# Kernel optimization log

Measured on AMD Instinct MI355X. Metric: run time of the kernel, lower is better.

The kernel has to match this reference:

```python
import jax, jax.numpy as jnp
import numpy as np

DIM = 2048
RANK = 128


def _xavier_uniform(key, shape, gain=0.5):
    fan_out, fan_in = shape
    limit = gain * np.sqrt(6.0 / (fan_in + fan_out))
    return jax.random.uniform(key, shape, jnp.float32, -limit, limit)


def setup_inputs() -> dict:
    key = jax.random.key(0)
    ks = jax.random.split(key, 6)
    T, B = 1024, 16
    x = jax.random.normal(ks[0], (T, B, DIM), jnp.float32)
    h0 = jax.random.normal(ks[1], (B, DIM), jnp.float32)
    U_x = _xavier_uniform(ks[2], (DIM, RANK))
    V_x = _xavier_uniform(ks[3], (RANK, DIM))
    U_d = _xavier_uniform(ks[4], (DIM, RANK))
    V_d = _xavier_uniform(ks[5], (RANK, DIM))
    r_h = jnp.full((DIM,), 0.9, jnp.float32)
    r_delta = jnp.full((DIM,), 0.1, jnp.float32)
    b = jnp.zeros((DIM,), jnp.float32)
    b_delta = jnp.full((DIM,), -2.0, jnp.float32)
    b_gate = jnp.zeros((DIM,), jnp.float32)
    return {"x": x, "h0": h0, "U_x": U_x, "V_x": V_x, "U_d": U_d, "V_d": V_d,
            "r_h": r_h, "r_delta": r_delta, "b": b, "b_delta": b_delta, "b_gate": b_gate}


def reference(x, h0, U_x, V_x, U_d, V_d, r_h, r_delta, b, b_delta, b_gate):
    # Precompute input projections for all timesteps (batched low-rank GEMMs):
    # W(x) = U @ (V @ x)  ->  [T,B,D]
    wx = jnp.einsum('tbd,rd,or->tbo', x, V_x, U_x)
    wd = jnp.einsum('tbd,rd,or->tbo', x, V_d, U_d)

    def step(h_prev, inp):
        x_t, wx_t, wd_t = inp
        cand = jnp.tanh(r_h * h_prev + wx_t + b)
        delta = jax.nn.sigmoid(wd_t + r_delta * h_prev + b_delta)
        h_new = (1.0 - delta) * h_prev + delta * cand
        g = h_new + x_t + b_gate
        out = h_new * (g * jax.nn.sigmoid(g))  # silu gate
        return h_new, (out, h_new)

    _, (output, hs) = jax.lax.scan(step, h0, (x, wx, wd))
    h = jnp.concatenate([h0[None], hs], axis=0)  # [T+1,B,D]
    return output, h
```

## Files before the change

### kernel.cpp

```cpp
#include <hip/hip_runtime.h>

#define DIMN 2048
#define RANKN 128
#define TT 1024
#define BBATCH 16
#define BD (BBATCH * DIMN)
#define CH 16
#define NCH (TT / CH)
#define PITW 66
#define PITH 36

typedef __attribute__((ext_vector_type(4))) float floatx4;
typedef __attribute__((ext_vector_type(8))) short short8;

__device__ __forceinline__ short f2bf(float f) {
    unsigned u = __float_as_uint(f);
    unsigned r = (u + 0x7FFFu + ((u >> 16) & 1u)) >> 16;
    return (short)r;
}
__device__ __forceinline__ float fast_sigmoid(float z) {
    return __builtin_amdgcn_rcpf(1.0f + __expf(-z));
}
__device__ __forceinline__ float fast_tanh(float z) {
    return 1.0f - 2.0f * __builtin_amdgcn_rcpf(__expf(2.0f * z) + 1.0f);
}

__global__ __launch_bounds__(256)
void prep_vb(const float* __restrict__ Vx, const float* __restrict__ Vd,
             short* __restrict__ Vb) {
    const int gid = blockIdx.x * 256 + threadIdx.x;
    const size_t base = (size_t)gid * 8;
    const size_t half = (size_t)RANKN * DIMN;
    const float* src = (base < half) ? Vx : Vd;
    const size_t off = (base < half) ? base : (base - half);
    float4 a = *(const float4*)(src + off);
    float4 c = *(const float4*)(src + off + 4);
    short8 v;
    v[0] = f2bf(a.x); v[1] = f2bf(a.y); v[2] = f2bf(a.z); v[3] = f2bf(a.w);
    v[4] = f2bf(c.x); v[5] = f2bf(c.y); v[6] = f2bf(c.z); v[7] = f2bf(c.w);
    *(short8*)(Vb + base) = v;
}

__global__ __launch_bounds__(256, 2)
void gemm_xv(const float* __restrict__ X, const short* __restrict__ Vb,
             short* __restrict__ xvb) {
    constexpr int PADK = 40;
    __shared__ short As[32 * PADK];
    __shared__ short Bs[2][128 * PADK];

    const int m0 = blockIdx.x * 32;
    const int tid = threadIdx.x;
    const int wave = tid >> 6;
    const int lane = tid & 63;
    const int lr = lane & 15;
    const int q  = lane >> 4;
    const int mat = wave >> 1;
    const int wn  = (wave & 1) * 64;

    floatx4 acc[2][4] = {};

    for (int k0 = 0; k0 < DIMN; k0 += 32) {
        {
            int r = tid >> 3, c = (tid & 7) * 4;
            float4 v = *(const float4*)(X + (size_t)(m0 + r) * DIMN + k0 + c);
            *(short4*)&As[r * PADK + c] =
                make_short4(f2bf(v.x), f2bf(v.y), f2bf(v.z), f2bf(v.w));
        }
        #pragma unroll
        for (int i = 0; i < 4; ++i) {
            int u = tid + i * 256;
            int bm = u >> 9;
            int rem = u & 511;
            int r = rem >> 2, c8 = (rem & 3) * 8;
            short8 v = *(const short8*)(Vb + ((size_t)bm * RANKN + r) * DIMN + k0 + c8);
            *(short8*)&Bs[bm][r * PADK + c8] = v;
        }
        __syncthreads();

        short8 af[2], bfr[4];
        #pragma unroll
        for (int mi = 0; mi < 2; ++mi)
            af[mi] = *(const short8*)&As[(mi * 16 + lr) * PADK + q * 8];
        #pragma unroll
        for (int nj = 0; nj < 4; ++nj)
            bfr[nj] = *(const short8*)&Bs[mat][(wn + nj * 16 + lr) * PADK + q * 8];

        #pragma unroll
        for (int mi = 0; mi < 2; ++mi)
            #pragma unroll
            for (int nj = 0; nj < 4; ++nj)
                acc[mi][nj] = __builtin_amdgcn_mfma_f32_16x16x32_bf16(
                    af[mi], bfr[nj], acc[mi][nj], 0, 0, 0);
        __syncthreads();
    }

    #pragma unroll
    for (int mi = 0; mi < 2; ++mi)
        #pragma unroll
        for (int nj = 0; nj < 4; ++nj)
            #pragma unroll
            for (int r = 0; r < 4; ++r) {
                int row = m0 + mi * 16 + q * 4 + r;
                int col = mat * RANKN + wn + nj * 16 + lr;
                xvb[(size_t)row * 256 + col] = f2bf(acc[mi][nj][r]);
            }
}

#define SPIN(ctr, tgt) \
    while (((volatile int*)cnt)[ctr] < (tgt)) __builtin_amdgcn_s_sleep(1); \
    asm volatile("" ::: "memory");

#define SIGNAL(ctr, val) \
    asm volatile("" ::: "memory"); \
    if (lane == 0) ((volatile int*)cnt)[ctr] = (val);

#define SIGNAL_AFTER_READS(ctr, val) \
    asm volatile("s_waitcnt lgkmcnt(0)" ::: "memory"); \
    if (lane == 0) ((volatile int*)cnt)[ctr] = (val);

__global__ __launch_bounds__(192, 3)
void fused_scan(const short* __restrict__ xvb, const float* __restrict__ x,
                const float* __restrict__ h0,
                const float* __restrict__ Ux, const float* __restrict__ Ud,
                const float* __restrict__ r_h, const float* __restrict__ r_delta,
                const float* __restrict__ bvec, const float* __restrict__ b_delta,
                const float* __restrict__ b_gate,
                float* __restrict__ obuf, float* __restrict__ hbuf) {
    __shared__ float wwds[4 * CH * PITW];
    __shared__ float hsd [4 * CH * PITH];
    __shared__ int cnt[4];

    const int id   = blockIdx.x;
    const int xcd  = id & 7;
    const int slot = id >> 3;
    const int b  = xcd * 2 + (slot & 1);
    const int d0 = (slot >> 1) * 32;

    const int tid  = threadIdx.x;
    const int wave = tid >> 6;
    const int lane = tid & 63;
    const int lr = lane & 15;
    const int q  = lane >> 4;

    if (tid == 0) { cnt[0] = 0; cnt[1] = 0; cnt[2] = 0; cnt[3] = 0; }
    __syncthreads();

    if (wave == 1) {
        short8 uf[2][2][4];
        #pragma unroll
        for (int mat = 0; mat < 2; ++mat) {
            const float* Up = mat ? Ud : Ux;
            #pragma unroll
            for (int nj = 0; nj < 2; ++nj) {
                const size_t dd = (size_t)(d0 + nj * 16 + lr);
                #pragma unroll
                for (int ks = 0; ks < 4; ++ks) {
                    const int k = ks * 32 + q * 8;
                    float4 u0 = *(const float4*)&Up[dd * RANKN + k];
                    float4 u1 = *(const float4*)&Up[dd * RANKN + k + 4];
                    short8 v;
                    v[0] = f2bf(u0.x); v[1] = f2bf(u0.y);
                    v[2] = f2bf(u0.z); v[3] = f2bf(u0.w);
                    v[4] = f2bf(u1.x); v[5] = f2bf(u1.y);
                    v[6] = f2bf(u1.z); v[7] = f2bf(u1.w);
                    uf[mat][nj][ks] = v;
                }
            }
        }
        short8 afp[2][4];
        {
            const size_t row = (size_t)lr * BBATCH + b;
            #pragma unroll
            for (int mat = 0; mat < 2; ++mat)
                #pragma unroll
                for (int ks = 0; ks < 4; ++ks)
                    afp[mat][ks] = *(const short8*)
                        &xvb[row * 256 + mat * RANKN + ks * 32 + q * 8];
        }
        for (int ch = 0; ch < NCH; ++ch) {
            if (ch >= 4) { SPIN(1, ch - 3) }
            const int sl = ch & 3;
            #pragma unroll
            for (int mat = 0; mat < 2; ++mat)
                #pragma unroll
                for (int nj = 0; nj < 2; ++nj) {
                    floatx4 acc = {};
                    #pragma unroll
                    for (int ks = 0; ks < 4; ++ks)
                        acc = __builtin_amdgcn_mfma_f32_16x16x32_bf16(
                            afp[mat][ks], uf[mat][nj][ks], acc, 0, 0, 0);
                    #pragma unroll
                    for (int r = 0; r < 4; ++r)
                        wwds[sl * (CH * PITW) + (q * 4 + r) * PITW
                             + (nj * 16 + lr) * 2 + mat] = acc[r];
                }
            SIGNAL(0, ch + 1)
            if (ch < NCH - 1) {
                const size_t row = (size_t)((ch + 1) * CH + lr) * BBATCH + b;
                #pragma unroll
                for (int mat = 0; mat < 2; ++mat)
                    #pragma unroll
                    for (int ks = 0; ks < 4; ++ks)
                        afp[mat][ks] = *(const short8*)
                            &xvb[row * 256 + mat * RANKN + ks * 32 + q * 8];
            }
        }
    } else if (wave == 0) {
        const int dcol = lane & 31;
        const int d = d0 + dcol;
        const size_t xo = (size_t)b * DIMN + d;
        const float rh  = r_h[d];
        const float rd  = r_delta[d];
        const float bb  = bvec[d];
        const float bdl = b_delta[d];
        float h = h0[xo];

        for (int ch = 0; ch < NCH; ++ch) {
            SPIN(0, ch + 1)
            const int sl = ch & 3;
            float2 wv[CH];
            #pragma unroll
            for (int s = 0; s < CH; ++s)
                wv[s] = *(const float2*)
                    &wwds[sl * (CH * PITW) + s * PITW + dcol * 2];
            SIGNAL_AFTER_READS(1, ch + 1)
            if (ch >= 4) { SPIN(3, ch - 3) }
            #pragma unroll
            for (int s = 0; s < CH; ++s) {
                const float cand  = fast_tanh(rh * h + wv[s].x + bb);
                const float delta = fast_sigmoid(wv[s].y + rd * h + bdl);
                h = (1.0f - delta) * h + delta * cand;
                hsd[sl * (CH * PITH) + s * PITH + dcol] = h;
            }
            SIGNAL(2, ch + 1)
        }
    } else {
        const int dq  = lane & 7;
        const int tof = lane >> 3;
        const size_t xoffF = (size_t)b * DIMN + d0 + dq * 4;
        const float4 bg4 = *(const float4*)&b_gate[d0 + dq * 4];
        if (tof == 0) {
            float4 hv = *(const float4*)&h0[xoffF];
            *(float4*)&hbuf[xoffF] = hv;
        }
        float4 xpre[2];
        #pragma unroll
        for (int jj = 0; jj < 2; ++jj)
            xpre[jj] = *(const float4*)&x[(size_t)(jj * 8 + tof) * BD + xoffF];

        for (int ch = 0; ch < NCH; ++ch) {
            SPIN(2, ch + 1)
            const int sl = ch & 3;
            float4 hv[2];
            #pragma unroll
            for (int jj = 0; jj < 2; ++jj)
                hv[jj] = *(const float4*)
                    &hsd[sl * (CH * PITH) + (jj * 8 + tof) * PITH + dq * 4];
            SIGNAL_AFTER_READS(3, ch + 1)
            const int tb = ch * CH;
            #pragma unroll
            for (int jj = 0; jj < 2; ++jj) {
                const int t = jj * 8 + tof;
                const float4 xv = xpre[jj];
                float4 ov;
                float g0 = hv[jj].x + xv.x + bg4.x;
                ov.x = hv[jj].x * (g0 * fast_sigmoid(g0));
                float g1 = hv[jj].y + xv.y + bg4.y;
                ov.y = hv[jj].y * (g1 * fast_sigmoid(g1));
                float g2 = hv[jj].z + xv.z + bg4.z;
                ov.z = hv[jj].z * (g2 * fast_sigmoid(g2));
                float g3 = hv[jj].w + xv.w + bg4.w;
                ov.w = hv[jj].w * (g3 * fast_sigmoid(g3));
                *(float4*)&obuf[(size_t)(tb + t) * BD + xoffF] = ov;
                *(float4*)&hbuf[(size_t)(tb + t + 1) * BD + xoffF] = hv[jj];
            }
            if (ch < NCH - 1) {
                const int tn = (ch + 1) * CH;
                #pragma unroll
                for (int jj = 0; jj < 2; ++jj)
                    xpre[jj] = *(const float4*)
                        &x[(size_t)(tn + jj * 8 + tof) * BD + xoffF];
            }
        }
    }
}

extern "C" void kernel_launch(void* const* d_in, const int* in_sizes, int n_in,
                              void* d_out, int out_size, void* d_ws, size_t ws_size,
                              hipStream_t stream) {
    const float* x       = (const float*)d_in[0];
    const float* h0      = (const float*)d_in[1];
    const float* U_x     = (const float*)d_in[2];
    const float* V_x     = (const float*)d_in[3];
    const float* U_d     = (const float*)d_in[4];
    const float* V_d     = (const float*)d_in[5];
    const float* r_h     = (const float*)d_in[6];
    const float* r_delta = (const float*)d_in[7];
    const float* bvec    = (const float*)d_in[8];
    const float* b_delta = (const float*)d_in[9];
    const float* b_gate  = (const float*)d_in[10];

    float* obuf = (float*)d_out;
    float* hbuf = obuf + (size_t)TT * BD;
    short* xvb  = (short*)d_ws;
    short* Vb   = xvb + (size_t)TT * BBATCH * 256;

    prep_vb<<<256, 256, 0, stream>>>(V_x, V_d, Vb);

    gemm_xv<<<TT * BBATCH / 32, 256, 0, stream>>>(x, Vb, xvb);

    fused_scan<<<1024, 192, 0, stream>>>(xvb, x, h0, U_x, U_d,
                                         r_h, r_delta, bvec, b_delta, b_gate,
                                         obuf, hbuf);
}
```

Baseline: 539.4 us.

## Double-buffer scan prefetches, widen GEMM K-tile, and busy-spin without sleep

The GEMM now stages a 64-wide K slice per iteration, with larger padding, so it needs half as many barrier pairs. In the fused scan, the projection wave and the output wave keep two chunks of global loads in flight through A/B register buffers, which gives more latency hiding. Spin-waits drop s_sleep to cut wake-up latency on the serial chain. The occupancy hint falls from 3 to 2 blocks per SM, which allows more registers per thread for the extra buffers but may reduce residency, and the tight spin may contend for issue slots.

After: 506.5 us. 6.1% less time.

```diff
diff --git a/kernel.cpp b/kernel.cpp
--- a/kernel.cpp
+++ b/kernel.cpp
@@ -44,7 +44,7 @@
 __global__ __launch_bounds__(256, 2)
 void gemm_xv(const float* __restrict__ X, const short* __restrict__ Vb,
              short* __restrict__ xvb) {
-    constexpr int PADK = 40;
+    constexpr int PADK = 72;
     __shared__ short As[32 * PADK];
     __shared__ short Bs[2][128 * PADK];
 
@@ -59,38 +59,46 @@
 
     floatx4 acc[2][4] = {};
 
-    for (int k0 = 0; k0 < DIMN; k0 += 32) {
-        {
-            int r = tid >> 3, c = (tid & 7) * 4;
+    for (int k0 = 0; k0 < DIMN; k0 += 64) {
+        #pragma unroll
+        for (int i = 0; i < 2; ++i) {
+            int f = tid + i * 256;
+            int r = f >> 4, c = (f & 15) * 4;
             float4 v = *(const float4*)(X + (size_t)(m0 + r) * DIMN + k0 + c);
             *(short4*)&As[r * PADK + c] =
                 make_short4(f2bf(v.x), f2bf(v.y), f2bf(v.z), f2bf(v.w));
         }
         #pragma unroll
-        for (int i = 0; i < 4; ++i) {
+        for (int i = 0; i < 8; ++i) {
             int u = tid + i * 256;
-            int bm = u >> 9;
-            int rem = u & 511;
-            int r = rem >> 2, c8 = (rem & 3) * 8;
+            int bm = u >> 10;
+            int rem = u & 1023;
+            int r = rem >> 3, c8 = (rem & 7) * 8;
             short8 v = *(const short8*)(Vb + ((size_t)bm * RANKN + r) * DIMN + k0 + c8);
             *(short8*)&Bs[bm][r * PADK + c8] = v;
         }
         __syncthreads();
 
-        short8 af[2], bfr[4];
-        #pragma unroll
-        for (int mi = 0; mi < 2; ++mi)
-            af[mi] = *(const short8*)&As[(mi * 16 + lr) * PADK + q * 8];
-        #pragma unroll
-        for (int nj = 0; nj < 4; ++nj)
-            bfr[nj] = *(const short8*)&Bs[mat][(wn + nj * 16 + lr) * PADK + q * 8];
-
-        #pragma unroll
-        for (int mi = 0; mi < 2; ++mi)
+        short8 af[2][2], bfr[2][4];
+        #pragma unroll
+        for (int kh = 0; kh < 2; ++kh) {
+            #pragma unroll
+            for (int mi = 0; mi < 2; ++mi)
+                af[kh][mi] = *(const short8*)
+                    &As[(mi * 16 + lr) * PADK + kh * 32 + q * 8];
             #pragma unroll
             for (int nj = 0; nj < 4; ++nj)
-                acc[mi][nj] = __builtin_amdgcn_mfma_f32_16x16x32_bf16(
-                    af[mi], bfr[nj], acc[mi][nj], 0, 0, 0);
+                bfr[kh][nj] = *(const short8*)
+                    &Bs[mat][(wn + nj * 16 + lr) * PADK + kh * 32 + q * 8];
+        }
+        #pragma unroll
+        for (int kh = 0; kh < 2; ++kh)
+            #pragma unroll
+            for (int mi = 0; mi < 2; ++mi)
+                #pragma unroll
+                for (int nj = 0; nj < 4; ++nj)
+                    acc[mi][nj] = __builtin_amdgcn_mfma_f32_16x16x32_bf16(
+                        af[kh][mi], bfr[kh][nj], acc[mi][nj], 0, 0, 0);
         __syncthreads();
     }
 
@@ -107,7 +115,7 @@
 }
 
 #define SPIN(ctr, tgt) \
-    while (((volatile int*)cnt)[ctr] < (tgt)) __builtin_amdgcn_s_sleep(1); \
+    while (((volatile int*)cnt)[ctr] < (tgt)) {} \
     asm volatile("" ::: "memory");
 
 #define SIGNAL(ctr, val) \
@@ -118,7 +126,7 @@
     asm volatile("s_waitcnt lgkmcnt(0)" ::: "memory"); \
     if (lane == 0) ((volatile int*)cnt)[ctr] = (val);
 
-__global__ __launch_bounds__(192, 3)
+__global__ __launch_bounds__(192, 2)
 void fused_scan(const short* __restrict__ xvb, const float* __restrict__ x,
                 const float* __restrict__ h0,
                 const float* __restrict__ Ux, const float* __restrict__ Ud,
@@ -167,18 +175,17 @@
                 }
             }
         }
-        short8 afp[2][4];
-        {
-            const size_t row = (size_t)lr * BBATCH + b;
+        short8 afA[2][4], afB[2][4];
+        auto ldaf = [&](int ch, short8 (&af)[2][4]) {
+            const size_t row = (size_t)(ch * CH + lr) * BBATCH + b;
             #pragma unroll
             for (int mat = 0; mat < 2; ++mat)
                 #pragma unroll
                 for (int ks = 0; ks < 4; ++ks)
-                    afp[mat][ks] = *(const short8*)
+                    af[mat][ks] = *(const short8*)
                         &xvb[row * 256 + mat * RANKN + ks * 32 + q * 8];
-        }
-        for (int ch = 0; ch < NCH; ++ch) {
-            if (ch >= 4) { SPIN(1, ch - 3) }
+        };
+        auto fill = [&](int ch, short8 (&af)[2][4]) {
             const int sl = ch & 3;
             #pragma unroll
             for (int mat = 0; mat < 2; ++mat)
@@ -188,22 +195,24 @@
                     #pragma unroll
                     for (int ks = 0; ks < 4; ++ks)
                         acc = __builtin_amdgcn_mfma_f32_16x16x32_bf16(
-                            afp[mat][ks], uf[mat][nj][ks], acc, 0, 0, 0);
+                            af[mat][ks], uf[mat][nj][ks], acc, 0, 0, 0);
                     #pragma unroll
                     for (int r = 0; r < 4; ++r)
                         wwds[sl * (CH * PITW) + (q * 4 + r) * PITW
                              + (nj * 16 + lr) * 2 + mat] = acc[r];
                 }
+        };
+        ldaf(0, afA);
+        ldaf(1, afB);
+        for (int ch = 0; ch < NCH; ch += 2) {
+            if (ch >= 4) { SPIN(1, ch - 3) }
+            fill(ch, afA);
             SIGNAL(0, ch + 1)
-            if (ch < NCH - 1) {
-                const size_t row = (size_t)((ch + 1) * CH + lr) * BBATCH + b;
-                #pragma unroll
-                for (int mat = 0; mat < 2; ++mat)
-                    #pragma unroll
-                    for (int ks = 0; ks < 4; ++ks)
-                        afp[mat][ks] = *(const short8*)
-                            &xvb[row * 256 + mat * RANKN + ks * 32 + q * 8];
-            }
+            if (ch + 2 < NCH) ldaf(ch + 2, afA);
+            if (ch + 1 >= 4) { SPIN(1, ch - 2) }
+            fill(ch + 1, afB);
+            SIGNAL(0, ch + 2)
+            if (ch + 3 < NCH) ldaf(ch + 3, afB);
         }
     } else if (wave == 0) {
         const int dcol = lane & 31;
@@ -243,12 +252,15 @@
             float4 hv = *(const float4*)&h0[xoffF];
             *(float4*)&hbuf[xoffF] = hv;
         }
-        float4 xpre[2];
-        #pragma unroll
-        for (int jj = 0; jj < 2; ++jj)
-            xpre[jj] = *(const float4*)&x[(size_t)(jj * 8 + tof) * BD + xoffF];
-
-        for (int ch = 0; ch < NCH; ++ch) {
+        float4 xpA[2], xpB[2];
+        auto ldx = [&](int ch, float4 (&xp)[2]) {
+            const int tn = ch * CH;
+            #pragma unroll
+            for (int jj = 0; jj < 2; ++jj)
+                xp[jj] = *(const float4*)
+                    &x[(size_t)(tn + jj * 8 + tof) * BD + xoffF];
+        };
+        auto flush = [&](int ch, float4 (&xp)[2]) {
             SPIN(2, ch + 1)
             const int sl = ch & 3;
             float4 hv[2];
@@ -261,7 +273,7 @@
             #pragma unroll
             for (int jj = 0; jj < 2; ++jj) {
                 const int t = jj * 8 + tof;
-                const float4 xv = xpre[jj];
+                const float4 xv = xp[jj];
                 float4 ov;
                 float g0 = hv[jj].x + xv.x + bg4.x;
                 ov.x = hv[jj].x * (g0 * fast_sigmoid(g0));
@@ -274,13 +286,14 @@
                 *(float4*)&obuf[(size_t)(tb + t) * BD + xoffF] = ov;
                 *(float4*)&hbuf[(size_t)(tb + t + 1) * BD + xoffF] = hv[jj];
             }
-            if (ch < NCH - 1) {
-                const int tn = (ch + 1) * CH;
-                #pragma unroll
-                for (int jj = 0; jj < 2; ++jj)
-                    xpre[jj] = *(const float4*)
-                        &x[(size_t)(tn + jj * 8 + tof) * BD + xoffF];
-            }
+        };
+        ldx(0, xpA);
+        ldx(1, xpB);
+        for (int ch = 0; ch < NCH; ch += 2) {
+            flush(ch, xpA);
+            if (ch + 2 < NCH) ldx(ch + 2, xpA);
+            flush(ch + 1, xpB);
+            if (ch + 3 < NCH) ldx(ch + 3, xpB);
         }
     }
 }
```
